# Kernel tuning notes

Measured on AMD Instinct MI355X. Metric: run time of the kernel, lower is better.

The kernel has to match this reference:

```python
import jax, jax.numpy as jnp
import numpy as np

EPS = 1e-6
T = 10.0
STEPS = 3
BN_EPS = 1e-5

def _normalize(x, axis):
    n = jnp.sqrt(jnp.sum(x * x, axis=axis, keepdims=True))
    return x / jnp.maximum(n, EPS)

def _vq_step(X, D):
    # X: (B, d, n), D: (B, d, r)
    Dn = _normalize(D, 1)
    Xn = _normalize(X, 1)
    cos = jnp.einsum('bdr,bdn->brn', Dn, Xn)          # (B, r, n)
    C = jax.nn.softmax(cos / T, axis=1)               # softmax over r
    XCt = jnp.einsum('bdn,brn->bdr', X, C)            # (B, d, r)
    sums = jnp.maximum(jnp.sum(C, axis=2), EPS)       # (B, r)
    D2 = _normalize(XCt / sums[:, None, :], 1)
    Xbar = jnp.einsum('bdr,brn->bdn', D2, C)
    return D2, C, Xbar

def _ham_vq(X, D0):
    # K-1 steps without gradient tracking, final step with grad through X only
    Xs = jax.lax.stop_gradient(X)
    def body(D, _):
        D, _, _ = _vq_step(Xs, D)
        return D, None
    D, _ = jax.lax.scan(body, _normalize(D0, 1), None, length=STEPS - 1)
    D = jax.lax.stop_gradient(D)
    _, _, Xbar = _vq_step(X, D)
    return Xbar

def _conv1x1(x, w, b=None):
    y = jnp.einsum('oc,bchw->bohw', w, x)
    if b is not None:
        y = y + b[None, :, None, None]
    return y

def _bn(x, gamma, beta, mean, var):
    inv = gamma / jnp.sqrt(var + BN_EPS)
    return x * inv[None, :, None, None] + (beta - mean * inv)[None, :, None, None]


def setup_inputs() -> dict:
    key = jax.random.key(0)
    ks = jax.random.split(key, 16)
    B, Cin, H, W = 8, 512, 64, 64
    d_mid, r = 512, 64
    out_ch = 2 * d_mid  # dual
    sc = 0.02
    inp = {
        'z': jax.random.normal(ks[0], (B, Cin, H, W), jnp.float32),
        'lower_w': jax.random.normal(ks[1], (out_ch, Cin), jnp.float32) * sc,
        'lower_b': jnp.zeros((out_ch,), jnp.float32),
        'Dinit_s': jax.random.uniform(ks[2], (B, d_mid, r), jnp.float32),
        'Dinit_c': jax.random.uniform(ks[3], (B, d_mid, r), jnp.float32),
        'cheese_w': jax.random.normal(ks[4], (out_ch, out_ch), jnp.float32) * sc,
        'ch_gamma': jnp.ones((out_ch,), jnp.float32),
        'ch_beta': jnp.zeros((out_ch,), jnp.float32),
        'ch_mean': jax.random.normal(ks[5], (out_ch,), jnp.float32) * 0.1,
        'ch_var': jax.random.uniform(ks[6], (out_ch,), jnp.float32) + 0.5,
        'upper_w': jax.random.normal(ks[7], (Cin, out_ch), jnp.float32) * sc,
        'upper_b': jnp.zeros((Cin,), jnp.float32),
        'h_gamma': jnp.ones((Cin,), jnp.float32),
        'h_beta': jnp.zeros((Cin,), jnp.float32),
        'h_mean': jax.random.normal(ks[8], (Cin,), jnp.float32) * 0.1,
        'h_var': jax.random.uniform(ks[9], (Cin,), jnp.float32) + 0.5,
        'coef_ham': jnp.array(1.0, jnp.float32),
        'coef_shortcut': jnp.array(1.0, jnp.float32),
    }
    return inp


def reference(z, lower_w, lower_b, Dinit_s, Dinit_c, cheese_w,
              ch_gamma, ch_beta, ch_mean, ch_var, upper_w, upper_b,
              h_gamma, h_beta, h_mean, h_var, coef_ham, coef_shortcut):
    B, Cin, H, W = z.shape
    identity = z
    # lower: conv1x1 + relu
    y = jax.nn.relu(_conv1x1(z, lower_w, lower_b))       # (B, 2*d_mid, H, W)
    d_mid = y.shape[1] // 2
    y1, y2 = y[:, :d_mid], y[:, d_mid:]
    n = H * W
    # spatial ham
    Xs = y1.reshape(B, d_mid, n)
    y1 = _ham_vq(Xs, Dinit_s).reshape(B, d_mid, H, W)
    # channel ham (same (B, d, n) flattening; HamMD requires dim1 == d_mid)
    Xc = y2.reshape(B, d_mid, n)
    y2 = _ham_vq(Xc, Dinit_c).reshape(B, d_mid, H, W)
    y = jnp.concatenate([y1, y2], axis=1)
    # cheese: conv1x1(no bias) + BN + relu
    y = jax.nn.relu(_bn(_conv1x1(y, cheese_w), ch_gamma, ch_beta, ch_mean, ch_var))
    # upper conv1x1 + BN
    h = _bn(_conv1x1(y, upper_w, upper_b), h_gamma, h_beta, h_mean, h_var)
    out = coef_ham * h + coef_shortcut * identity
    return jax.nn.relu(out)
```

## Files before the change

### kernel.cpp

```cpp
#include <hip/hip_runtime.h>
#include <hip/hip_bf16.h>

typedef __bf16 bf16_t;
typedef __bf16 bf16x4 __attribute__((ext_vector_type(4)));
typedef __bf16 bf16x8 __attribute__((ext_vector_type(8)));
typedef float  f32x4  __attribute__((ext_vector_type(4)));

#define HEPS 1e-6f

__device__ __forceinline__ void gload16(const bf16_t* g, bf16_t* l) {
    __builtin_amdgcn_global_load_lds(
        (const __attribute__((address_space(1))) unsigned int*)(g),
        (__attribute__((address_space(3))) unsigned int*)(l),
        16, 0, 0);
}


__global__ void cvt_f32_bf16_k(const float* __restrict__ src, bf16_t* __restrict__ dst, int n) {
    int i = blockIdx.x * 256 + threadIdx.x;
    if (i < n) dst[i] = (bf16_t)src[i];
}

__global__ void prep_k(const float* __restrict__ chg, const float* __restrict__ chb,
                       const float* __restrict__ chm, const float* __restrict__ chv,
                       const float* __restrict__ hg, const float* __restrict__ hb,
                       const float* __restrict__ hm, const float* __restrict__ hv,
                       const float* __restrict__ ub, const float* __restrict__ cham,
                       float* __restrict__ chA, float* __restrict__ chB,
                       float* __restrict__ hA2, float* __restrict__ hB2) {
    int i = blockIdx.x * 256 + threadIdx.x;
    if (i < 1024) {
        float inv = chg[i] * rsqrtf(chv[i] + 1e-5f);
        chA[i] = inv;
        chB[i] = chb[i] - chm[i] * inv;
    }
    if (i < 512) {
        float inv = hg[i] * rsqrtf(hv[i] + 1e-5f);
        float cA = cham[0];
        hA2[i] = cA * inv;
        hB2[i] = cA * (fmaf(ub[i], inv, hb[i]) - hm[i] * inv);
    }
}

__global__ void tz_k(const float* __restrict__ z, bf16_t* __restrict__ Zt) {
    __shared__ bf16_t t[64][68];
    int b = blockIdx.z, kt = blockIdx.y, nt = blockIdx.x;
    const float* src = z + ((size_t)b * 512 + kt * 64) * 4096 + nt * 64;
    int tid = threadIdx.x;
    int kr = tid >> 4;
    int nc = (tid & 15) * 4;
    #pragma unroll
    for (int it = 0; it < 4; ++it) {
        int k = kr + it * 16;
        float4 v = *(const float4*)&src[(size_t)k * 4096 + nc];
        t[nc + 0][k] = (bf16_t)v.x; t[nc + 1][k] = (bf16_t)v.y;
        t[nc + 2][k] = (bf16_t)v.z; t[nc + 3][k] = (bf16_t)v.w;
    }
    __syncthreads();
    bf16_t* dst = Zt + ((size_t)b * 4096 + nt * 64) * 512 + kt * 64;
    int nr = tid >> 4;
    int kc = (tid & 15) * 4;
    #pragma unroll
    for (int it = 0; it < 4; ++it) {
        int n = nr + it * 16;
        bf16x4 o;
        #pragma unroll
        for (int c = 0; c < 4; ++c) o[c] = t[n][kc + c];
        *(bf16x4*)&dst[(size_t)n * 512 + kc] = o;
    }
}

__global__ void dinit_k(const float* __restrict__ Ds, const float* __restrict__ Dc,
                        bf16_t* __restrict__ Dt) {
    int bs = blockIdx.y;
    int b = bs >> 1;
    const float* src = ((bs & 1) ? Dc : Ds) + (size_t)b * 512 * 64;
    int idx = blockIdx.x * 256 + threadIdx.x;
    int r = idx & 63, d = idx >> 6;
    Dt[(size_t)bs * 64 * 512 + (size_t)r * 512 + d] = (bf16_t)src[d * 64 + r];
}

__global__ void dnorm_k(const bf16_t* __restrict__ Dt, float* __restrict__ dinv) {
    int gw = (blockIdx.x * 256 + threadIdx.x) >> 6;
    int lane = threadIdx.x & 63;
    bf16x8 v = *(const bf16x8*)(Dt + (size_t)gw * 512 + lane * 8);
    float s = 0.f;
    #pragma unroll
    for (int e = 0; e < 8; ++e) { float f = (float)v[e]; s += f * f; }
    #pragma unroll
    for (int off = 32; off > 0; off >>= 1) s += __shfl_xor(s, off);
    if (lane == 0) dinv[gw] = 1.0f / fmaxf(sqrtf(s), HEPS);
}

__global__ void reduce_k(const float* __restrict__ P, bf16_t* __restrict__ Dt,
                         float* __restrict__ dinv) {
    int bsr = blockIdx.x;
    int bs = bsr >> 6, r = bsr & 63;
    int lane = threadIdx.x;
    const float* base = P + ((size_t)(bs * 4) * 64 + r) * 512 + lane * 8;
    float s[8] = {0.f, 0.f, 0.f, 0.f, 0.f, 0.f, 0.f, 0.f};
    #pragma unroll
    for (int kc = 0; kc < 4; ++kc) {
        const float* p = base + (size_t)kc * 64 * 512;
        float4 u = *(const float4*)p;
        float4 w = *(const float4*)(p + 4);
        s[0] += u.x; s[1] += u.y; s[2] += u.z; s[3] += u.w;
        s[4] += w.x; s[5] += w.y; s[6] += w.z; s[7] += w.w;
    }
    bf16x8 o;
    float sq = 0.f;
    #pragma unroll
    for (int e = 0; e < 8; ++e) { sq += s[e] * s[e]; o[e] = (bf16_t)s[e]; }
    *(bf16x8*)&Dt[(size_t)bsr * 512 + lane * 8] = o;
    #pragma unroll
    for (int off = 32; off > 0; off >>= 1) sq += __shfl_xor(sq, off);
    if (lane == 0) dinv[bsr] = 1.0f / fmaxf(sqrtf(sq), HEPS);
}

template<int BM, int BN, int WAVES_M, int WAVES_N, int EPI, int ORDER>
__launch_bounds__(256)
__global__ void g2(const bf16_t* __restrict__ Ag, const bf16_t* __restrict__ Bg,
                   void* __restrict__ Cg, void* __restrict__ C2g,
                   const int M, const int N, const int K,
                   const int ldA, const int ldB, const int ldC,
                   const long aStride, const long bStride,
                   const long cStride, const long c2Stride,
                   const float* __restrict__ p0, const float* __restrict__ p1,
                   const float* __restrict__ scal,
                   const void* __restrict__ shortcut, const long sStride)
{
    constexpr int WM = BM / WAVES_M, WN = BN / WAVES_N;
    constexpr int FM = WM / 16, FN = WN / 16;
    constexpr int ASEG = BM / 64, BSEG = BN / 64;
    constexpr int LPT = ASEG + BSEG;

    __shared__ __align__(64) bf16_t SH[3 * (BM + BN) * 32];
    __shared__ float dl[64];
    bf16_t* Al = SH;
    bf16_t* Bl = SH + 3 * BM * 32;

    const int tid = threadIdx.x;
    const int wave = tid >> 6, lane = tid & 63;
    const int l15 = lane & 15, q = lane >> 4;
    const int lrow = lane >> 2, lcol = (lane & 3) * 8;

    const int gx = gridDim.x, gy = gridDim.y;
    const int per = gx * gy;
    const int nwg = per * gridDim.z;
    const int g = blockIdx.z * per + blockIdx.y * gx + blockIdx.x;
    const int qq = nwg >> 3, rr = nwg & 7;
    const int xcd = g & 7, jj = g >> 3;
    const int w = (xcd < rr ? xcd * (qq + 1) : rr * (qq + 1) + (xcd - rr) * qq) + jj;
    const int bz = w / per;
    const int rem = w - bz * per;
    int bx, by;
    if constexpr (ORDER == 0) { by = rem / gx; bx = rem - by * gx; }
    else                      { bx = rem / gy; by = rem - bx * gy; }

    int bs = bz, exA = 0, exB = 0;
    if constexpr (EPI == 5) { bs = bz >> 2; exA = exB = (bz & 3) * 1024; }
    if constexpr (EPI == 7) { exA = (bz & 1) * 512; }

    const int n0 = bx * BN;
    const int m0 = by * BM;
    const int wm0 = (wave / WAVES_N) * WM;
    const int wn0 = (wave % WAVES_N) * WN;

    const bf16_t* Ab = Ag + (size_t)bs * (size_t)aStride + exA;
    const bf16_t* Bb;
    if constexpr (EPI == 6)
        Bb = Bg + (size_t)(bz >> 1) * (size_t)bStride + (size_t)(bz & 1) * 512;
    else
        Bb = Bg + (size_t)bs * (size_t)bStride + exB;

    if constexpr (EPI == 6) { if (tid < 64) dl[tid] = p0[bz * 64 + tid]; }

    auto stage = [&](int buf, int k0) {
        #pragma unroll
        for (int t = 0; t < ASEG; ++t) {
            int seg = wave * ASEG + t;
            gload16(Ab + (size_t)(m0 + seg * 16 + lrow) * ldA + k0 + lcol,
                    &Al[buf * BM * 32 + seg * 512]);
        }
        #pragma unroll
        for (int t = 0; t < BSEG; ++t) {
            int seg = wave * BSEG + t;
            gload16(Bb + (size_t)(n0 + seg * 16 + lrow) * ldB + k0 + lcol,
                    &Bl[buf * BN * 32 + seg * 512]);
        }
    };

    f32x4 acc[FM][FN];
    #pragma unroll
    for (int i = 0; i < FM; ++i)
        #pragma unroll
        for (int j = 0; j < FN; ++j)
            #pragma unroll
            for (int e = 0; e < 4; ++e) acc[i][j][e] = 0.f;

    float xsq[FN];
    #pragma unroll
    for (int j = 0; j < FN; ++j) xsq[j] = 0.f;

    const int nK = K / 32;
    stage(0, 0);
    if (nK > 1) stage(1, 32);

    for (int t = 0; t < nK; ++t) {
        const int cur = t % 3;

        if (t < nK - 1) asm volatile("s_waitcnt vmcnt(%0)" :: "i"(LPT) : "memory");
        else            asm volatile("s_waitcnt vmcnt(0)" ::: "memory");
        asm volatile("s_barrier" ::: "memory");
        __builtin_amdgcn_sched_barrier(0);

        if (t + 2 < nK) stage((t + 2) % 3, (t + 2) * 32);

        bf16x8 af[FM], bfm[FN];
        #pragma unroll
        for (int i = 0; i < FM; ++i)
            af[i] = *(const bf16x8*)&Al[cur * BM * 32 + (wm0 + 16 * i + l15) * 32 + 8 * q];
        #pragma unroll
        for (int j = 0; j < FN; ++j)
            bfm[j] = *(const bf16x8*)&Bl[cur * BN * 32 + (wn0 + 16 * j + l15) * 32 + 8 * q];

        if constexpr (EPI == 6) {
            #pragma unroll
            for (int j = 0; j < FN; ++j)
                #pragma unroll
                for (int e = 0; e < 8; ++e) {
                    float f = (float)bfm[j][e];
                    xsq[j] = fmaf(f, f, xsq[j]);
                }
        }

        __builtin_amdgcn_s_setprio(1);
        #pragma unroll
        for (int i = 0; i < FM; ++i)
            #pragma unroll
            for (int j = 0; j < FN; ++j)
                acc[i][j] = __builtin_amdgcn_mfma_f32_16x16x32_bf16(af[i], bfm[j], acc[i][j], 0, 0, 0);
        __builtin_amdgcn_s_setprio(0);
    }

    int rowB[FM];
    #pragma unroll
    for (int i = 0; i < FM; ++i) rowB[i] = m0 + wm0 + 16 * i + 4 * q;
    const int colBase = n0 + wn0;

    if constexpr (EPI == 2) {
        bf16_t* O = (bf16_t*)Cg + (size_t)bz * (size_t)cStride;
        #pragma unroll
        for (int j = 0; j < FN; ++j) {
            int col = colBase + 16 * j + l15;
            float a = p0[col], b = p1[col];
            #pragma unroll
            for (int i = 0; i < FM; ++i) {
                int rb = rowB[i];
                #pragma unroll
                for (int e = 0; e < 4; ++e) {
                    float v = fmaxf(fmaf(acc[i][j][e], a, b), 0.f);
                    O[(size_t)(rb + e) * ldC + col] = (bf16_t)v;
                }
            }
        }
    } else if constexpr (EPI == 3) {
        float* O = (float*)Cg + (size_t)bz * (size_t)cStride;
        const float* sc = (const float*)shortcut + (size_t)bz * (size_t)sStride;
        float cB = scal[0];
        #pragma unroll
        for (int i = 0; i < FM; ++i) {
            int rb = rowB[i];
            #pragma unroll
            for (int e = 0; e < 4; ++e) {
                int row = rb + e;
                float a = p0[row], b = p1[row];
                #pragma unroll
                for (int j = 0; j < FN; ++j) {
                    int col = colBase + 16 * j + l15;
                    float v = fmaf(acc[i][j][e], a, b) + cB * sc[(size_t)row * ldC + col];
                    O[(size_t)row * ldC + col] = fmaxf(v, 0.f);
                }
            }
        }
    } else if constexpr (EPI == 5) {
        float* O = (float*)Cg + (size_t)bz * (size_t)cStride;
        #pragma unroll
        for (int i = 0; i < FM; ++i) {
            int rb = rowB[i];
            #pragma unroll
            for (int j = 0; j < FN; ++j) {
                int col = colBase + 16 * j + l15;
                *(f32x4*)&O[(size_t)col * ldC + rb] = acc[i][j];
            }
        }
    } else if constexpr (EPI == 6) {
        bf16_t* Cc = (bf16_t*)Cg  + (size_t)bz * (size_t)cStride;
        bf16_t* Ct = (bf16_t*)C2g + (size_t)(bz >> 1) * (size_t)c2Stride;
        const int hoff = (bz & 1) * 64;
        const bool doCt = (C2g != nullptr);
        #pragma unroll
        for (int j = 0; j < FN; ++j) {
            int col = colBase + 16 * j + l15;
            float s2 = xsq[j];
            s2 += __shfl_xor(s2, 16);
            s2 += __shfl_xor(s2, 32);
            float xi = 1.0f / (10.0f * fmaxf(sqrtf(s2), HEPS));
            float mx = -1e30f;
            #pragma unroll
            for (int i = 0; i < FM; ++i)
                #pragma unroll
                for (int e = 0; e < 4; ++e) {
                    float v = acc[i][j][e] * dl[rowB[i] + e] * xi;
                    acc[i][j][e] = v;
                    mx = fmaxf(mx, v);
                }
            mx = fmaxf(mx, __shfl_xor(mx, 16));
            mx = fmaxf(mx, __shfl_xor(mx, 32));
            float sm = 0.f;
            #pragma unroll
            for (int i = 0; i < FM; ++i)
                #pragma unroll
                for (int e = 0; e < 4; ++e) {
                    float p = __expf(acc[i][j][e] - mx);
                    acc[i][j][e] = p;
                    sm += p;
                }
            sm += __shfl_xor(sm, 16);
            sm += __shfl_xor(sm, 32);
            float rs = 1.0f / sm;
            #pragma unroll
            for (int i = 0; i < FM; ++i) {
                int rb = rowB[i];
                bf16x4 t;
                #pragma unroll
                for (int e = 0; e < 4; ++e) {
                    t[e] = (bf16_t)(acc[i][j][e] * rs);
                    Cc[(size_t)(rb + e) * ldC + col] = t[e];
                }
                if (doCt) *(bf16x4*)&Ct[(size_t)col * 128 + hoff + rb] = t;
            }
        }
    } else if constexpr (EPI == 7) {
        bf16_t* O = (bf16_t*)Cg + (size_t)(bz >> 1) * (size_t)cStride;
        const int hoff = (bz & 1) * 64;
        #pragma unroll
        for (int j = 0; j < FN; ++j) {
            int col = colBase + 16 * j + l15;
            float di = p0[bz * 64 + col];
            #pragma unroll
            for (int i = 0; i < FM; ++i) {
                int rb = rowB[i];
                #pragma unroll
                for (int e = 0; e < 4; ++e)
                    O[(size_t)(rb + e) * 128 + hoff + col] = (bf16_t)(acc[i][j][e] * di);
            }
        }
    } else if constexpr (EPI == 8) {
        bf16_t* O  = (bf16_t*)Cg  + (size_t)bz * (size_t)cStride;
        bf16_t* O2 = (bf16_t*)C2g + (size_t)bz * (size_t)c2Stride;
        #pragma unroll
        for (int j = 0; j < FN; ++j) {
            int col = colBase + 16 * j + l15;
            float bias = p0[col];
            #pragma unroll
            for (int i = 0; i < FM; ++i) {
                int rb = rowB[i];
                bf16x4 t;
                #pragma unroll
                for (int e = 0; e < 4; ++e) {
                    float v = fmaxf(acc[i][j][e] + bias, 0.f);
                    t[e] = (bf16_t)v;
                    O[(size_t)(rb + e) * ldC + col] = t[e];
                }
                *(bf16x4*)&O2[(size_t)col * 4096 + rb] = t;
            }
        }
    }
}


extern "C" void kernel_launch(void* const* d_in, const int* in_sizes, int n_in,
                              void* d_out, int out_size, void* d_ws, size_t ws_size,
                              hipStream_t stream) {
    const float* z        = (const float*)d_in[0];
    const float* lower_w  = (const float*)d_in[1];
    const float* lower_b  = (const float*)d_in[2];
    const float* Dinit_s  = (const float*)d_in[3];
    const float* Dinit_c  = (const float*)d_in[4];
    const float* cheese_w = (const float*)d_in[5];
    const float* ch_gamma = (const float*)d_in[6];
    const float* ch_beta  = (const float*)d_in[7];
    const float* ch_mean  = (const float*)d_in[8];
    const float* ch_var   = (const float*)d_in[9];
    const float* upper_w  = (const float*)d_in[10];
    const float* upper_b  = (const float*)d_in[11];
    const float* h_gamma  = (const float*)d_in[12];
    const float* h_beta   = (const float*)d_in[13];
    const float* h_mean   = (const float*)d_in[14];
    const float* h_var    = (const float*)d_in[15];
    const float* coef_ham = (const float*)d_in[16];
    const float* coef_sc  = (const float*)d_in[17];

    char* ws = (char*)d_ws;
    size_t off = 0;
    auto alloc = [&](size_t bytes) -> void* {
        void* p = ws + off;
        off += (bytes + 255) & ~(size_t)255;
        return p;
    };

    bf16_t* Wl   = (bf16_t*)alloc((size_t)1024 * 512 * 2);
    bf16_t* Wc   = (bf16_t*)alloc((size_t)1024 * 1024 * 2);
    bf16_t* Wu   = (bf16_t*)alloc((size_t)512 * 1024 * 2);
    float*  chA  = (float*) alloc(1024 * 4);
    float*  chB  = (float*) alloc(1024 * 4);
    float*  hA2  = (float*) alloc(512 * 4);
    float*  hB2  = (float*) alloc(512 * 4);
    float*  dinv = (float*) alloc(1024 * 4);
    bf16_t* Xbf  = (bf16_t*)alloc((size_t)8 * 1024 * 4096 * 2);
    bf16_t* Xt   = (bf16_t*)alloc((size_t)8 * 4096 * 1024 * 2);
    bf16_t* Zt   = (bf16_t*)alloc((size_t)8 * 4096 * 512 * 2);
    bf16_t* Cb   = (bf16_t*)alloc((size_t)16 * 64 * 4096 * 2);
    bf16_t* Ct2  = (bf16_t*)alloc((size_t)8 * 4096 * 128 * 2);
    float*  P    = (float*) alloc((size_t)64 * 64 * 512 * 4);
    bf16_t* Dta  = (bf16_t*)alloc((size_t)16 * 64 * 512 * 2);
    bf16_t* Dtb  = (bf16_t*)alloc((size_t)16 * 64 * 512 * 2);
    bf16_t* Eb   = (bf16_t*)alloc((size_t)8 * 1024 * 128 * 2);
    bf16_t* Ycht = Xbf;

    dim3 blk(256);

    cvt_f32_bf16_k<<<2048, blk, 0, stream>>>(lower_w, Wl, 1024 * 512);
    cvt_f32_bf16_k<<<4096, blk, 0, stream>>>(cheese_w, Wc, 1024 * 1024);
    cvt_f32_bf16_k<<<2048, blk, 0, stream>>>(upper_w, Wu, 512 * 1024);
    prep_k<<<4, blk, 0, stream>>>(ch_gamma, ch_beta, ch_mean, ch_var,
                                  h_gamma, h_beta, h_mean, h_var,
                                  upper_b, coef_ham, chA, chB, hA2, hB2);
    tz_k<<<dim3(64, 8, 8), blk, 0, stream>>>(z, Zt);
    dinit_k<<<dim3(128, 16), blk, 0, stream>>>(Dinit_s, Dinit_c, Dta);

    g2<128, 128, 2, 2, 8, 0><<<dim3(8, 32, 8), blk, 0, stream>>>(
        Zt, Wl, (void*)Xt, (void*)Xbf, 4096, 1024, 512,
        512, 512, 1024,
        (long)4096 * 512, 0L, (long)4096 * 1024, (long)1024 * 4096,
        lower_b, nullptr, nullptr, nullptr, 0L);

    dnorm_k<<<256, blk, 0, stream>>>(Dta, dinv);

    bf16_t* cur = Dta;
    bf16_t* nxt = Dtb;
    for (int t = 0; t < 3; ++t) {
        g2<64, 256, 1, 4, 6, 0><<<dim3(16, 1, 16), blk, 0, stream>>>(
            cur, Xt, (void*)Cb, (t == 2) ? (void*)Ct2 : nullptr, 64, 4096, 512,
            512, 1024, 4096,
            (long)64 * 512, (long)4096 * 1024, (long)64 * 4096, (long)4096 * 128,
            dinv, nullptr, nullptr, nullptr, 0L);
        g2<128, 64, 2, 2, 5, 0><<<dim3(1, 4, 64), blk, 0, stream>>>(
            Xbf, Cb, (void*)P, nullptr, 512, 64, 1024,
            4096, 4096, 512,
            (long)512 * 4096, (long)64 * 4096, (long)64 * 512, 0L,
            nullptr, nullptr, nullptr, nullptr, 0L);
        reduce_k<<<1024, dim3(64), 0, stream>>>(P, nxt, dinv);
        bf16_t* tmp = cur; cur = nxt; nxt = tmp;
    }

    g2<128, 64, 2, 2, 7, 0><<<dim3(1, 8, 16), blk, 0, stream>>>(
        Wc, cur, (void*)Eb, nullptr, 1024, 64, 512,
        1024, 512, 128,
        0L, (long)64 * 512, (long)1024 * 128, 0L,
        dinv, nullptr, nullptr, nullptr, 0L);

    g2<128, 128, 2, 2, 2, 0><<<dim3(8, 32, 8), blk, 0, stream>>>(
        Ct2, Eb, (void*)Ycht, nullptr, 4096, 1024, 128,
        128, 128, 1024,
        (long)4096 * 128, (long)1024 * 128, (long)4096 * 1024, 0L,
        chA, chB, nullptr, nullptr, 0L);

    g2<128, 128, 2, 2, 3, 1><<<dim3(32, 4, 8), blk, 0, stream>>>(
        Wu, Ycht, d_out, nullptr, 512, 4096, 1024,
        1024, 1024, 4096,
        0L, (long)4096 * 1024, (long)512 * 4096, 0L,
        hA2, hB2, coef_sc, z, (long)512 * 4096);

    (void)in_sizes; (void)n_in; (void)out_size; (void)ws_size;
}
```

Before: 317.6 us.

## Transpose cosine-softmax GEMM orientation and merge weight conversion kernels

```diff
diff --git a/kernel.cpp b/kernel.cpp
--- a/kernel.cpp
+++ b/kernel.cpp
@@ -16,9 +16,13 @@
 }
 
 
-__global__ void cvt_f32_bf16_k(const float* __restrict__ src, bf16_t* __restrict__ dst, int n) {
+__global__ void cvt_all_k(const float* __restrict__ wl, bf16_t* __restrict__ dwl,
+                          const float* __restrict__ wc, bf16_t* __restrict__ dwc,
+                          const float* __restrict__ wu, bf16_t* __restrict__ dwu) {
     int i = blockIdx.x * 256 + threadIdx.x;
-    if (i < n) dst[i] = (bf16_t)src[i];
+    if (i < 524288) dwl[i] = (bf16_t)wl[i];
+    else if (i < 1572864) { int k = i - 524288; dwc[k] = (bf16_t)wc[k]; }
+    else { int k = i - 1572864; dwu[k] = (bf16_t)wu[k]; }
 }
 
 __global__ void prep_k(const float* __restrict__ chg, const float* __restrict__ chb,
@@ -166,12 +170,15 @@
     const int wm0 = (wave / WAVES_N) * WM;
     const int wn0 = (wave % WAVES_N) * WN;
 
-    const bf16_t* Ab = Ag + (size_t)bs * (size_t)aStride + exA;
+    const bf16_t* Ab;
     const bf16_t* Bb;
-    if constexpr (EPI == 6)
-        Bb = Bg + (size_t)(bz >> 1) * (size_t)bStride + (size_t)(bz & 1) * 512;
-    else
+    if constexpr (EPI == 6) {
+        Ab = Ag + (size_t)(bz >> 1) * (size_t)aStride + (size_t)(bz & 1) * 512;
+        Bb = Bg + (size_t)bz * (size_t)bStride;
+    } else {
+        Ab = Ag + (size_t)bs * (size_t)aStride + exA;
         Bb = Bg + (size_t)bs * (size_t)bStride + exB;
+    }
 
     if constexpr (EPI == 6) { if (tid < 64) dl[tid] = p0[bz * 64 + tid]; }
 
@@ -198,9 +205,9 @@
             #pragma unroll
             for (int e = 0; e < 4; ++e) acc[i][j][e] = 0.f;
 
-    float xsq[FN];
-    #pragma unroll
-    for (int j = 0; j < FN; ++j) xsq[j] = 0.f;
+    float xsq[FM];
+    #pragma unroll
+    for (int i = 0; i < FM; ++i) xsq[i] = 0.f;
 
     const int nK = K / 32;
     stage(0, 0);
@@ -226,11 +233,11 @@
 
         if constexpr (EPI == 6) {
             #pragma unroll
-            for (int j = 0; j < FN; ++j)
+            for (int i = 0; i < FM; ++i)
                 #pragma unroll
                 for (int e = 0; e < 8; ++e) {
-                    float f = (float)bfm[j][e];
-                    xsq[j] = fmaf(f, f, xsq[j]);
+                    float f = (float)af[i][e];
+                    xsq[i] = fmaf(f, f, xsq[i]);
                 }
         }
 
@@ -299,47 +306,54 @@
         bf16_t* Ct = (bf16_t*)C2g + (size_t)(bz >> 1) * (size_t)c2Stride;
         const int hoff = (bz & 1) * 64;
         const bool doCt = (C2g != nullptr);
-        #pragma unroll
-        for (int j = 0; j < FN; ++j) {
-            int col = colBase + 16 * j + l15;
-            float s2 = xsq[j];
+        float xs[FM];
+        #pragma unroll
+        for (int i = 0; i < FM; ++i) {
+            float s2 = xsq[i];
             s2 += __shfl_xor(s2, 16);
             s2 += __shfl_xor(s2, 32);
-            float xi = 1.0f / (10.0f * fmaxf(sqrtf(s2), HEPS));
-            float mx = -1e30f;
-            #pragma unroll
-            for (int i = 0; i < FM; ++i)
-                #pragma unroll
-                for (int e = 0; e < 4; ++e) {
-                    float v = acc[i][j][e] * dl[rowB[i] + e] * xi;
-                    acc[i][j][e] = v;
-                    mx = fmaxf(mx, v);
-                }
-            mx = fmaxf(mx, __shfl_xor(mx, 16));
-            mx = fmaxf(mx, __shfl_xor(mx, 32));
-            float sm = 0.f;
-            #pragma unroll
-            for (int i = 0; i < FM; ++i)
-                #pragma unroll
-                for (int e = 0; e < 4; ++e) {
-                    float p = __expf(acc[i][j][e] - mx);
-                    acc[i][j][e] = p;
-                    sm += p;
-                }
-            sm += __shfl_xor(sm, 16);
-            sm += __shfl_xor(sm, 32);
-            float rs = 1.0f / sm;
-            #pragma unroll
-            for (int i = 0; i < FM; ++i) {
-                int rb = rowB[i];
-                bf16x4 t;
-                #pragma unroll
-                for (int e = 0; e < 4; ++e) {
-                    t[e] = (bf16_t)(acc[i][j][e] * rs);
-                    Cc[(size_t)(rb + e) * ldC + col] = t[e];
-                }
-                if (doCt) *(bf16x4*)&Ct[(size_t)col * 128 + hoff + rb] = t;
-            }
+            xs[i] = s2;
+        }
+        float di[FN];
+        #pragma unroll
+        for (int j = 0; j < FN; ++j) di[j] = dl[16 * j + l15];
+        #pragma unroll
+        for (int i = 0; i < FM; ++i) {
+            int rb = rowB[i];
+            bf16x4 tj[FN];
+            #pragma unroll
+            for (int e = 0; e < 4; ++e) {
+                float s2row = __shfl(xs[i], 4 * q + e);
+                float xi = 1.0f / (10.0f * fmaxf(sqrtf(s2row), HEPS));
+                float v[FN];
+                float mx = -1e30f;
+                #pragma unroll
+                for (int j = 0; j < FN; ++j) {
+                    v[j] = acc[i][j][e] * di[j] * xi;
+                    mx = fmaxf(mx, v[j]);
+                }
+                mx = fmaxf(mx, __shfl_xor(mx, 1));
+                mx = fmaxf(mx, __shfl_xor(mx, 2));
+                mx = fmaxf(mx, __shfl_xor(mx, 4));
+                mx = fmaxf(mx, __shfl_xor(mx, 8));
+                float sm = 0.f;
+                #pragma unroll
+                for (int j = 0; j < FN; ++j) { v[j] = __expf(v[j] - mx); sm += v[j]; }
+                sm += __shfl_xor(sm, 1);
+                sm += __shfl_xor(sm, 2);
+                sm += __shfl_xor(sm, 4);
+                sm += __shfl_xor(sm, 8);
+                float rs = 1.0f / sm;
+                #pragma unroll
+                for (int j = 0; j < FN; ++j) {
+                    float p = v[j] * rs;
+                    tj[j][e] = (bf16_t)p;
+                    if (doCt) Ct[(size_t)(rb + e) * 128 + hoff + 16 * j + l15] = (bf16_t)p;
+                }
+            }
+            #pragma unroll
+            for (int j = 0; j < FN; ++j)
+                *(bf16x4*)&Cc[(size_t)(16 * j + l15) * ldC + rb] = tj[j];
         }
     } else if constexpr (EPI == 7) {
         bf16_t* O = (bf16_t*)Cg + (size_t)(bz >> 1) * (size_t)cStride;
@@ -431,9 +445,7 @@
 
     dim3 blk(256);
 
-    cvt_f32_bf16_k<<<2048, blk, 0, stream>>>(lower_w, Wl, 1024 * 512);
-    cvt_f32_bf16_k<<<4096, blk, 0, stream>>>(cheese_w, Wc, 1024 * 1024);
-    cvt_f32_bf16_k<<<2048, blk, 0, stream>>>(upper_w, Wu, 512 * 1024);
+    cvt_all_k<<<8192, blk, 0, stream>>>(lower_w, Wl, cheese_w, Wc, upper_w, Wu);
     prep_k<<<4, blk, 0, stream>>>(ch_gamma, ch_beta, ch_mean, ch_var,
                                   h_gamma, h_beta, h_mean, h_var,
                                   upper_b, coef_ham, chA, chB, hA2, hB2);
@@ -451,10 +463,10 @@
     bf16_t* cur = Dta;
     bf16_t* nxt = Dtb;
     for (int t = 0; t < 3; ++t) {
-        g2<64, 256, 1, 4, 6, 0><<<dim3(16, 1, 16), blk, 0, stream>>>(
-            cur, Xt, (void*)Cb, (t == 2) ? (void*)Ct2 : nullptr, 64, 4096, 512,
-            512, 1024, 4096,
-            (long)64 * 512, (long)4096 * 1024, (long)64 * 4096, (long)4096 * 128,
+        g2<256, 64, 4, 1, 6, 0><<<dim3(1, 16, 16), blk, 0, stream>>>(
+            Xt, cur, (void*)Cb, (t == 2) ? (void*)Ct2 : nullptr, 4096, 64, 512,
+            1024, 512, 4096,
+            (long)4096 * 1024, (long)64 * 512, (long)64 * 4096, (long)4096 * 128,
             dinv, nullptr, nullptr, nullptr, 0L);
         g2<128, 64, 2, 2, 5, 0><<<dim3(1, 4, 64), blk, 0, stream>>>(
             Xbf, Cb, (void*)P, nullptr, 512, 64, 1024,
```

Result: slower. 329.8 us (+3.8%).
